# Kernel tuning notes

Measured on AMD Instinct MI355X. Metric: run time of the kernel, lower is better.

The kernel has to match this reference:

```python
import jax, jax.numpy as jnp
import numpy as np

Z, Y, X = 32, 480, 480          # sparse voxel grid (LiDAR-scale)
N = 200_000                     # active voxels
C_IN, C_OUT = 64, 64
EPS = 1e-5


def _subm_conv(f, nbr, w):
    """Submanifold sparse conv as gather-matmul-accumulate.
    f: [N, Cin]; nbr: [N, K] neighbor row ids, pad index == N for missing;
    w: [K, Cin, Cout]."""
    f_pad = jnp.concatenate([f, jnp.zeros((1, f.shape[1]), f.dtype)], axis=0)
    g = f_pad[nbr]                       # [N, K, Cin] gathered neighbor features
    return jnp.einsum('nkc,kco->no', g, w)


def _bn(x, gamma, beta):
    # BatchNorm1d in training mode: batch stats over the N dimension
    m = x.mean(axis=0)
    v = x.var(axis=0)
    return (x - m) * jax.lax.rsqrt(v + EPS) * gamma + beta


def setup_inputs() -> dict:
    rng = np.random.default_rng(0)
    ids = rng.choice(Z * Y * X, size=N, replace=False)
    lookup = np.full(Z * Y * X, -1, dtype=np.int64)
    lookup[ids] = np.arange(N)
    z = ids // (Y * X)
    y = (ids // X) % Y
    x = ids % X

    def nbr_table(offsets):
        cols = []
        for dz, dy, dx in offsets:
            zz, yy, xx = z + dz, y + dy, x + dx
            ok = (zz >= 0) & (zz < Z) & (yy >= 0) & (yy < Y) & (xx >= 0) & (xx < X)
            lin = np.clip((zz * Y + yy) * X + xx, 0, Z * Y * X - 1)
            idx = np.where(ok, lookup[lin], -1)
            cols.append(np.where(idx >= 0, idx, N))   # pad index N -> zero row
        return jnp.asarray(np.stack(cols, axis=1).astype(np.int32))

    off13 = [(0, dy, dx) for dy in (-1, 0, 1) for dx in (-1, 0, 1)]  # kernel (1,3,3)
    off31 = [(dz, 0, dx) for dz in (-1, 0, 1) for dx in (-1, 0, 1)]  # kernel (3,1,3)

    key = jax.random.key(0)
    ks = jax.random.split(key, 5)
    s = 0.05
    ones = jnp.ones((C_OUT,), jnp.float32)
    zeros = jnp.zeros((C_OUT,), jnp.float32)
    return {
        'features': jax.random.normal(ks[0], (N, C_IN), jnp.float32),
        'w1':   jax.random.normal(ks[1], (9, C_IN, C_OUT), jnp.float32) * s,
        'w1_2': jax.random.normal(ks[2], (9, C_OUT, C_OUT), jnp.float32) * s,
        'w2':   jax.random.normal(ks[3], (9, C_IN, C_OUT), jnp.float32) * s,
        'w3':   jax.random.normal(ks[4], (9, C_OUT, C_OUT), jnp.float32) * s,
        'g0': ones, 'b0': zeros, 'g0_2': ones, 'b0_2': zeros,
        'g1': ones, 'b1': zeros, 'g2': ones, 'b2': zeros,
        'nbr13': nbr_table(off13),
        'nbr31': nbr_table(off31),
    }


def reference(features, w1, w1_2, w2, w3, g0, b0, g0_2, b0_2, g1, b1, g2, b2,
              nbr13, nbr31):
    # shortcut branch: conv1x3 -> LeakyReLU -> BN -> conv3x1 -> LeakyReLU -> BN
    sc = _subm_conv(features, nbr13, w1)
    sc = _bn(jax.nn.leaky_relu(sc), g0, b0)
    sc = _subm_conv(sc, nbr31, w1_2)
    sc = _bn(jax.nn.leaky_relu(sc), g0_2, b0_2)
    # main branch: conv3x1 -> LeakyReLU -> BN -> conv1x3 -> LeakyReLU -> BN
    r = _subm_conv(features, nbr31, w2)
    r = _bn(jax.nn.leaky_relu(r), g1, b1)
    r = _subm_conv(r, nbr13, w3)
    r = _bn(jax.nn.leaky_relu(r), g2, b2)
    return r + sc
```

## Files before the change

kernel.cpp:

```cpp
#include <hip/hip_runtime.h>

#define NVOX 200000
#define TM 128
#define NBLK 1563
#define NREP 32
#define STG 4224

typedef unsigned short u16;
typedef unsigned int u32;
typedef __bf16 bf16x8 __attribute__((ext_vector_type(8)));
typedef float f32x16 __attribute__((ext_vector_type(16)));

__device__ __forceinline__ float bf2f(u16 h) { return __uint_as_float(((u32)h) << 16); }
__device__ __forceinline__ u16 f2bf(float x) {
  u32 u = __float_as_uint(x);
  u32 r = u + 0x7fffu + ((u >> 16) & 1u);
  return (u16)(r >> 16);
}
__device__ __forceinline__ uint4 cvt8(uint4 a, uint4 b) {
  const float* fa = (const float*)&a;
  const float* fb = (const float*)&b;
  uint4 r;
  u16* q = (u16*)&r;
#pragma unroll
  for (int j = 0; j < 4; ++j) { q[j] = f2bf(fa[j]); q[4 + j] = f2bf(fb[j]); }
  return r;
}

template <bool IN_F32, bool FOLDED, int MODE>
__global__ __launch_bounds__(256, 4)
void conv_k(const void* __restrict__ fv, const int* __restrict__ nbr,
            const u16* __restrict__ wf, void* yv, float* __restrict__ st,
            float* io, const float* __restrict__ affD,
            const float* __restrict__ affB) {
  __shared__ __align__(16) float fb[128 * 68];
  __shared__ float sred[4][128];

  const int tid = threadIdx.x;
  const int wv = tid >> 6;
  const int lane = tid & 63;
  const int lrow = lane & 31;
  const int lq = lane >> 5;
  const int base = blockIdx.x * TM;
  const int gr = base + wv * 32 + lrow;

  int ids[9];
#pragma unroll
  for (int j = 0; j < 9; ++j) ids[j] = (gr < NVOX) ? nbr[gr * 9 + j] : NVOX;

  f32x16 acc0 = {0.f, 0.f, 0.f, 0.f, 0.f, 0.f, 0.f, 0.f,
                 0.f, 0.f, 0.f, 0.f, 0.f, 0.f, 0.f, 0.f};
  f32x16 acc1 = acc0;
  constexpr int KSTRIDE = FOLDED ? 5120 : 4096;

#pragma unroll
  for (int k = 0; k < 9; ++k) {
    if (k != 4) {
      if (__ballot(ids[k] < NVOX) == 0ull) continue;
    }
    const int id = ids[k];
    const bool ok = id < NVOX;
    uint4 af[4];
    if constexpr (IN_F32) {
      const float* p = (const float*)fv + (size_t)id * 64 + lq * 8;
#pragma unroll
      for (int ksi = 0; ksi < 4; ++ksi) {
        uint4 v0 = make_uint4(0u, 0u, 0u, 0u), v1 = v0;
        if (ok) { v0 = *(const uint4*)(p + ksi * 16); v1 = *(const uint4*)(p + ksi * 16 + 4); }
        af[ksi] = cvt8(v0, v1);
      }
    } else {
      const u16* p = (const u16*)fv + (size_t)id * 64 + lq * 8;
#pragma unroll
      for (int ksi = 0; ksi < 4; ++ksi) {
        uint4 v = make_uint4(0u, 0u, 0u, 0u);
        if (ok) v = *(const uint4*)(p + ksi * 16);
        af[ksi] = v;
      }
    }
    const u16* wb = wf + k * KSTRIDE;
#pragma unroll
    for (int ksi = 0; ksi < 4; ++ksi) {
      bf16x8 a = __builtin_bit_cast(bf16x8, af[ksi]);
      bf16x8 b0 = __builtin_bit_cast(bf16x8, *(const uint4*)(wb + (ksi * 2) * 512 + lane * 8));
      bf16x8 b1 = __builtin_bit_cast(bf16x8, *(const uint4*)(wb + (ksi * 2 + 1) * 512 + lane * 8));
      acc0 = __builtin_amdgcn_mfma_f32_32x32x16_bf16(a, b0, acc0, 0, 0, 0);
      acc1 = __builtin_amdgcn_mfma_f32_32x32x16_bf16(a, b1, acc1, 0, 0, 0);
    }
    if constexpr (FOLDED) {
      uint4 a4 = make_uint4(0u, 0u, 0u, 0u);
      if (lq == 0 && ok) ((u16*)&a4)[0] = 0x3F80u;
      bf16x8 a = __builtin_bit_cast(bf16x8, a4);
      bf16x8 b0 = __builtin_bit_cast(bf16x8, *(const uint4*)(wb + 8 * 512 + lane * 8));
      bf16x8 b1 = __builtin_bit_cast(bf16x8, *(const uint4*)(wb + 9 * 512 + lane * 8));
      acc0 = __builtin_amdgcn_mfma_f32_32x32x16_bf16(a, b0, acc0, 0, 0, 0);
      acc1 = __builtin_amdgcn_mfma_f32_32x32x16_bf16(a, b1, acc1, 0, 0, 0);
    }
  }

  const int cc0 = lrow, cc1 = 32 + lrow;
  float aD0 = 0.f, aD1 = 0.f, hD0 = 0.f, hD1 = 0.f;
  if constexpr (MODE == 2) {
    aD0 = affD[cc0]; hD0 = affD[64 + cc0];
    aD1 = affD[cc1]; hD1 = affD[64 + cc1];
  }
  float s0 = 0.f, q0 = 0.f, s1 = 0.f, q1 = 0.f;
  float vout[2][16];
#pragma unroll
  for (int r = 0; r < 16; ++r) {
    float v = acc0[r]; v = v > 0.f ? v : 0.01f * v;
    s0 += v; q0 += v * v; vout[0][r] = v;
    float w = acc1[r]; w = w > 0.f ? w : 0.01f * w;
    s1 += w; q1 += w * w; vout[1][r] = w;
  }
  if constexpr (MODE != 2) {
    s0 += __shfl_xor(s0, 32); q0 += __shfl_xor(q0, 32);
    s1 += __shfl_xor(s1, 32); q1 += __shfl_xor(q1, 32);
    if (lq == 0) {
      sred[wv][lrow] = s0; sred[wv][32 + lrow] = s1;
      sred[wv][64 + lrow] = q0; sred[wv][96 + lrow] = q1;
    }
  }
  if constexpr (MODE == 0) {
    u16* bb = (u16*)fb;
#pragma unroll
    for (int r = 0; r < 16; ++r) {
      int rowD = 32 * wv + (r & 3) + 8 * (r >> 2) + 4 * lq;
      bb[rowD * 72 + cc0] = f2bf(vout[0][r]);
      bb[rowD * 72 + cc1] = f2bf(vout[1][r]);
    }
  } else if constexpr (MODE == 2 || MODE == 3) {
#pragma unroll
    for (int r = 0; r < 16; ++r) {
      int rowD = 32 * wv + (r & 3) + 8 * (r >> 2) + 4 * lq;
      float v0 = vout[0][r], v1 = vout[1][r];
      if constexpr (MODE == 2) { v0 = fmaf(v0, aD0, hD0); v1 = fmaf(v1, aD1, hD1); }
      fb[rowD * 68 + cc0] = v0;
      fb[rowD * 68 + cc1] = v1;
    }
  }
  __syncthreads();

  const int trow = tid >> 3, cp = tid & 7;
  if constexpr (MODE == 0) {
    u16* y = (u16*)yv;
    const u16* bb = (const u16*)fb;
#pragma unroll
    for (int it = 0; it < 4; ++it) {
      int r = it * 32 + trow, row = base + r;
      if (row < NVOX)
        *(uint4*)(y + (size_t)row * 64 + cp * 8) = *(const uint4*)(bb + r * 72 + cp * 8);
    }
  }
  if constexpr (MODE == 3) {
    float* y = (float*)yv;
#pragma unroll
    for (int it = 0; it < 4; ++it) {
      int r = it * 32 + trow, row = base + r;
      if (row < NVOX) {
        *(float4*)(y + (size_t)row * 64 + cp * 8) = *(const float4*)(fb + r * 68 + cp * 8);
        *(float4*)(y + (size_t)row * 64 + cp * 8 + 4) = *(const float4*)(fb + r * 68 + cp * 8 + 4);
      }
    }
  }
  if constexpr (MODE == 2) {
    float* y = (float*)yv;
#pragma unroll
    for (int it = 0; it < 4; ++it) {
      int r = it * 32 + trow, row = base + r;
      if (row < NVOX) {
        float t[8], p[8], o[8];
        *(float4*)&t[0] = *(const float4*)(fb + r * 68 + cp * 8);
        *(float4*)&t[4] = *(const float4*)(fb + r * 68 + cp * 8 + 4);
        *(float4*)&p[0] = *(const float4*)(io + (size_t)row * 64 + cp * 8);
        *(float4*)&p[4] = *(const float4*)(io + (size_t)row * 64 + cp * 8 + 4);
#pragma unroll
        for (int j = 0; j < 8; ++j) {
          int c = cp * 8 + j;
          o[j] = t[j] + fmaf(p[j], affB[c], affB[64 + c]);
        }
        *(float4*)(y + (size_t)row * 64 + cp * 8) = *(const float4*)&o[0];
        *(float4*)(y + (size_t)row * 64 + cp * 8 + 4) = *(const float4*)&o[4];
      }
    }
  }
  if constexpr (MODE != 2) {
    if (tid < 128) {
      int which = tid >> 6, c = tid & 63;
      float v = sred[0][which * 64 + c] + sred[1][which * 64 + c] +
                sred[2][which * 64 + c] + sred[3][which * 64 + c];
      atomicAdd(&st[(blockIdx.x & (NREP - 1)) * 128 + which * 64 + c], v);
    }
  }
}

__global__ void prep_all(const float* __restrict__ feat, const float* __restrict__ w1,
                         const float* __restrict__ w2, u16* __restrict__ wf,
                         u16* __restrict__ F, float* __restrict__ st, int cvt_blocks) {
  const int bid = blockIdx.x, tid = threadIdx.x;
  if (bid < cvt_blocks) {
    int i8 = (bid * 256 + tid) * 8;
    if (i8 < NVOX * 64) {
      uint4 a = *(const uint4*)(feat + i8);
      uint4 b = *(const uint4*)(feat + i8 + 4);
      *(uint4*)(F + i8) = cvt8(a, b);
    }
    return;
  }
  int rb = bid - cvt_blocks;
  if (rb < 288) {
    int e = rb * 256 + tid;
    int slot = e / 36864, r = e % 36864;
    int k = r >> 12, rr = r & 4095;
    int frag = rr >> 9, lane = (rr >> 3) & 63, j = rr & 7;
    int ks = frag >> 1, ct = frag & 1;
    int cin = ks * 16 + (lane >> 5) * 8 + j;
    int cout = ct * 32 + (lane & 31);
    const float* src = slot ? w2 : w1;
    wf[e] = f2bf(src[k * 4096 + cin * 64 + cout]);
    return;
  }
  for (int i = tid; i < 4 * STG; i += 256) st[i] = 0.f;
}

__global__ void wscale(const float* __restrict__ wraw, float* __restrict__ stp,
                       const float* __restrict__ g, const float* __restrict__ b,
                       u16* __restrict__ dst) {
  __shared__ float sc[64], sh[64];
  const int tid = threadIdx.x;
  if (tid < 64) {
    float s = 0.f, q = 0.f;
#pragma unroll
    for (int r = 0; r < NREP; ++r) {
      s += stp[r * 128 + tid];
      q += stp[r * 128 + 64 + tid];
    }
    const float invn = 1.0f / (float)NVOX;
    float mean = s * invn;
    float var = q * invn - mean * mean;
    float sca = g[tid] * rsqrtf(var + 1e-5f);
    sc[tid] = sca;
    sh[tid] = b[tid] - mean * sca;
    if (blockIdx.x == 0) { stp[4096 + tid] = sca; stp[4160 + tid] = sh[tid]; }
  }
  __syncthreads();
  int e = blockIdx.x * 256 + tid;
  int k = e / 5120, r = e % 5120;
  int frag = r >> 9, lane = (r >> 3) & 63, j = r & 7;
  int ks = frag >> 1, ct = frag & 1;
  int cout = ct * 32 + (lane & 31);
  u16 val = 0;
  if (ks < 4) {
    int cin = ks * 16 + (lane >> 5) * 8 + j;
    val = f2bf(sc[cin] * wraw[k * 4096 + cin * 64 + cout]);
  } else if (((lane >> 5) == 0) && j == 0) {
    float acc = 0.f;
    for (int c = 0; c < 64; ++c) acc += sh[c] * wraw[k * 4096 + c * 64 + cout];
    val = f2bf(acc);
  }
  dst[e] = val;
}

__global__ void finalize_bn(float* __restrict__ st, const float* __restrict__ g,
                            const float* __restrict__ b) {
  int c = threadIdx.x;
  if (c < 64) {
    float s = 0.f, q = 0.f;
#pragma unroll
    for (int r = 0; r < NREP; ++r) {
      s += st[r * 128 + c];
      q += st[r * 128 + 64 + c];
    }
    const float invn = 1.0f / (float)NVOX;
    float mean = s * invn;
    float var = q * invn - mean * mean;
    float sca = g[c] * rsqrtf(var + 1e-5f);
    st[4096 + c] = sca;
    st[4160 + c] = b[c] - mean * sca;
  }
}

__global__ void final_add(const u16* __restrict__ y3, float* io,
                          const float* __restrict__ affB, const float* __restrict__ affD) {
  int i8 = (blockIdx.x * 256 + threadIdx.x) * 8;
  if (i8 < NVOX * 64) {
    float a[8];
    *(float4*)&a[0] = *(const float4*)(io + i8);
    *(float4*)&a[4] = *(const float4*)(io + i8 + 4);
    uint4 vd = *(const uint4*)(y3 + i8);
    const u16* pd = (const u16*)&vd;
    int cb = i8 & 63;
    float o[8];
#pragma unroll
    for (int j = 0; j < 8; ++j) {
      int c = cb + j;
      o[j] = fmaf(a[j], affB[c], affB[64 + c]) + fmaf(bf2f(pd[j]), affD[c], affD[64 + c]);
    }
    *(float4*)(io + i8) = *(const float4*)&o[0];
    *(float4*)(io + i8 + 4) = *(const float4*)&o[4];
  }
}

extern "C" void kernel_launch(void* const* d_in, const int* in_sizes, int n_in,
                              void* d_out, int out_size, void* d_ws, size_t ws_size,
                              hipStream_t stream) {
  const float* feat = (const float*)d_in[0];
  const float* w1 = (const float*)d_in[1];
  const float* w1_2 = (const float*)d_in[2];
  const float* w2 = (const float*)d_in[3];
  const float* w3 = (const float*)d_in[4];
  const float* g0 = (const float*)d_in[5];
  const float* b0 = (const float*)d_in[6];
  const float* g0_2 = (const float*)d_in[7];
  const float* b0_2 = (const float*)d_in[8];
  const float* g1 = (const float*)d_in[9];
  const float* b1 = (const float*)d_in[10];
  const float* g2 = (const float*)d_in[11];
  const float* b2 = (const float*)d_in[12];
  const int* nbr13 = (const int*)d_in[13];
  const int* nbr31 = (const int*)d_in[14];
  float* out = (float*)d_out;

  char* ws = (char*)d_ws;
  float* st = (float*)ws;
  u16* wf = (u16*)(ws + 67584);
  u16* s0 = wf;
  u16* s1 = wf + 36864;
  u16* s2 = wf + 73728;
  u16* s3 = wf + 119808;
  u16* F = (u16*)(ws + 67584 + 331776);
  u16* A = F + (size_t)NVOX * 64;
  const size_t need_big = 67584 + 331776 + 2ull * NVOX * 64 * 2;
  const bool big = (ws_size >= need_big);

  float* st0 = st, *st1 = st + STG, *st2 = st + 2 * STG, *st3 = st + 3 * STG;

  if (big) {
    prep_all<<<6539, 256, 0, stream>>>(feat, w1, w2, wf, F, st, 6250);
    conv_k<false, false, 0><<<NBLK, 256, 0, stream>>>(F, nbr13, s0, A, st0, nullptr, nullptr, nullptr);
    wscale<<<180, 256, 0, stream>>>(w1_2, st0, g0, b0, s2);
    conv_k<false, true, 3><<<NBLK, 256, 0, stream>>>(A, nbr31, s2, out, st1, nullptr, nullptr, nullptr);
    conv_k<false, false, 0><<<NBLK, 256, 0, stream>>>(F, nbr31, s1, A, st2, nullptr, nullptr, nullptr);
    wscale<<<180, 256, 0, stream>>>(w3, st2, g1, b1, s3);
    conv_k<false, true, 0><<<NBLK, 256, 0, stream>>>(A, nbr13, s3, F, st3, nullptr, nullptr, nullptr);
    finalize_bn<<<1, 64, 0, stream>>>(st1, g0_2, b0_2);
    finalize_bn<<<1, 64, 0, stream>>>(st3, g2, b2);
    final_add<<<6250, 256, 0, stream>>>(F, out, st1 + 4096, st3 + 4096);
  } else {
    u16* Az = F;
    prep_all<<<289, 256, 0, stream>>>(feat, w1, w2, wf, nullptr, st, 0);
    conv_k<true, false, 0><<<NBLK, 256, 0, stream>>>(feat, nbr13, s0, Az, st0, nullptr, nullptr, nullptr);
    wscale<<<180, 256, 0, stream>>>(w1_2, st0, g0, b0, s2);
    conv_k<false, true, 3><<<NBLK, 256, 0, stream>>>(Az, nbr31, s2, out, st1, nullptr, nullptr, nullptr);
    finalize_bn<<<1, 64, 0, stream>>>(st1, g0_2, b0_2);
    conv_k<true, false, 0><<<NBLK, 256, 0, stream>>>(feat, nbr31, s1, Az, st2, nullptr, nullptr, nullptr);
    wscale<<<180, 256, 0, stream>>>(w3, st2, g1, b1, s3);
    conv_k<false, true, 1><<<NBLK, 256, 0, stream>>>(Az, nbr13, s3, nullptr, st3, nullptr, nullptr, nullptr);
    finalize_bn<<<1, 64, 0, stream>>>(st3, g2, b2);
    conv_k<false, true, 2><<<NBLK, 256, 0, stream>>>(Az, nbr13, s3, out, nullptr, out, st3 + 4096, st1 + 4096);
  }
}
```

Baseline: 287.6 us.

## Fuse independent branch convolutions into single launches with doubled grid

Adds a conv_fused kernel that runs the shortcut and main branch convolutions of the same stage in one launch, with blocks split by index between the two branches. It also merges the two weight-scaling kernels and the two BN finalizers, and doubles the stats replica count to spread atomic contention. The aim is fewer launches, more concurrent work per launch and less serialization between stages. The cost is a third activation buffer, a larger workspace, and a new fused kernel that drops early-exit and epilogue variants. The fallback paths call wscale2 with mismatched grid sizes and fragile ordering.

```diff
diff --git a/kernel.cpp b/kernel.cpp
--- a/kernel.cpp
+++ b/kernel.cpp
@@ -3,8 +3,8 @@
 #define NVOX 200000
 #define TM 128
 #define NBLK 1563
-#define NREP 32
-#define STG 4224
+#define NREP 64
+#define STG 8320
 
 typedef unsigned short u16;
 typedef unsigned int u32;
@@ -25,6 +25,142 @@
 #pragma unroll
   for (int j = 0; j < 4; ++j) { q[j] = f2bf(fa[j]); q[4 + j] = f2bf(fb[j]); }
   return r;
+}
+
+template <int PHASE>
+__global__ __launch_bounds__(256, 4)
+void conv_fused(const u16* __restrict__ inA, const u16* __restrict__ inB,
+                const int* __restrict__ nbrA, const int* __restrict__ nbrB,
+                const u16* __restrict__ wfA, const u16* __restrict__ wfB,
+                void* yA, void* yB, float* __restrict__ stA, float* __restrict__ stB) {
+  __shared__ __align__(16) float fb4[64 * 68];
+  __shared__ float sred[4][128];
+
+  const int tid = threadIdx.x;
+  const int bid = blockIdx.x;
+  const bool hB = (bid >= NBLK);
+  const int blk = hB ? bid - NBLK : bid;
+  const u16* f = hB ? inB : inA;
+  const int* nbr = hB ? nbrB : nbrA;
+  const u16* wf = hB ? wfB : wfA;
+  float* st = hB ? stB : stA;
+
+  const int wv = tid >> 6;
+  const int lane = tid & 63;
+  const int lrow = lane & 31;
+  const int lq = lane >> 5;
+  const int base = blk * TM;
+  const int gr = base + wv * 32 + lrow;
+
+  int ids[9];
+#pragma unroll
+  for (int j = 0; j < 9; ++j) ids[j] = (gr < NVOX) ? nbr[gr * 9 + j] : NVOX;
+
+  f32x16 acc0 = {0.f, 0.f, 0.f, 0.f, 0.f, 0.f, 0.f, 0.f,
+                 0.f, 0.f, 0.f, 0.f, 0.f, 0.f, 0.f, 0.f};
+  f32x16 acc1 = acc0;
+  constexpr bool FOLDED = (PHASE == 1);
+  constexpr int KSTRIDE = FOLDED ? 5120 : 4096;
+
+#pragma unroll
+  for (int k = 0; k < 9; ++k) {
+    if (k != 4) {
+      if (__ballot(ids[k] < NVOX) == 0ull) continue;
+    }
+    const int id = ids[k];
+    const bool ok = id < NVOX;
+    uint4 af[4];
+    const u16* p = f + (size_t)id * 64 + lq * 8;
+#pragma unroll
+    for (int ksi = 0; ksi < 4; ++ksi) {
+      uint4 v = make_uint4(0u, 0u, 0u, 0u);
+      if (ok) v = *(const uint4*)(p + ksi * 16);
+      af[ksi] = v;
+    }
+    const u16* wb = wf + k * KSTRIDE;
+#pragma unroll
+    for (int ksi = 0; ksi < 4; ++ksi) {
+      bf16x8 a = __builtin_bit_cast(bf16x8, af[ksi]);
+      bf16x8 b0 = __builtin_bit_cast(bf16x8, *(const uint4*)(wb + (ksi * 2) * 512 + lane * 8));
+      bf16x8 b1 = __builtin_bit_cast(bf16x8, *(const uint4*)(wb + (ksi * 2 + 1) * 512 + lane * 8));
+      acc0 = __builtin_amdgcn_mfma_f32_32x32x16_bf16(a, b0, acc0, 0, 0, 0);
+      acc1 = __builtin_amdgcn_mfma_f32_32x32x16_bf16(a, b1, acc1, 0, 0, 0);
+    }
+    if constexpr (FOLDED) {
+      uint4 a4 = make_uint4(0u, 0u, 0u, 0u);
+      if (lq == 0 && ok) ((u16*)&a4)[0] = 0x3F80u;
+      bf16x8 a = __builtin_bit_cast(bf16x8, a4);
+      bf16x8 b0 = __builtin_bit_cast(bf16x8, *(const uint4*)(wb + 8 * 512 + lane * 8));
+      bf16x8 b1 = __builtin_bit_cast(bf16x8, *(const uint4*)(wb + 9 * 512 + lane * 8));
+      acc0 = __builtin_amdgcn_mfma_f32_32x32x16_bf16(a, b0, acc0, 0, 0, 0);
+      acc1 = __builtin_amdgcn_mfma_f32_32x32x16_bf16(a, b1, acc1, 0, 0, 0);
+    }
+  }
+
+  const int cc0 = lrow, cc1 = 32 + lrow;
+  float s0 = 0.f, q0 = 0.f, s1 = 0.f, q1 = 0.f;
+  float vout[2][16];
+#pragma unroll
+  for (int r = 0; r < 16; ++r) {
+    float v = acc0[r]; v = v > 0.f ? v : 0.01f * v;
+    s0 += v; q0 += v * v; vout[0][r] = v;
+    float w = acc1[r]; w = w > 0.f ? w : 0.01f * w;
+    s1 += w; q1 += w * w; vout[1][r] = w;
+  }
+  s0 += __shfl_xor(s0, 32); q0 += __shfl_xor(q0, 32);
+  s1 += __shfl_xor(s1, 32); q1 += __shfl_xor(q1, 32);
+  if (lq == 0) {
+    sred[wv][lrow] = s0; sred[wv][32 + lrow] = s1;
+    sred[wv][64 + lrow] = q0; sred[wv][96 + lrow] = q1;
+  }
+
+  const bool f32out = (PHASE == 1) && !hB;
+  const int trow = tid >> 3, cp = tid & 7;
+  u16* bb = (u16*)fb4;
+#pragma unroll
+  for (int h = 0; h < 2; ++h) {
+    __syncthreads();
+    if ((wv >> 1) == h) {
+      const int lr = 32 * (wv & 1);
+#pragma unroll
+      for (int r = 0; r < 16; ++r) {
+        int rowD = lr + (r & 3) + 8 * (r >> 2) + 4 * lq;
+        if (f32out) {
+          fb4[rowD * 68 + cc0] = vout[0][r];
+          fb4[rowD * 68 + cc1] = vout[1][r];
+        } else {
+          bb[rowD * 72 + cc0] = f2bf(vout[0][r]);
+          bb[rowD * 72 + cc1] = f2bf(vout[1][r]);
+        }
+      }
+    }
+    __syncthreads();
+    if (f32out) {
+      float* y = (float*)yA;
+#pragma unroll
+      for (int it = 0; it < 2; ++it) {
+        int r = it * 32 + trow, row = base + 64 * h + r;
+        if (row < NVOX) {
+          *(float4*)(y + (size_t)row * 64 + cp * 8) = *(const float4*)(fb4 + r * 68 + cp * 8);
+          *(float4*)(y + (size_t)row * 64 + cp * 8 + 4) = *(const float4*)(fb4 + r * 68 + cp * 8 + 4);
+        }
+      }
+    } else {
+      u16* y = (u16*)(hB ? yB : yA);
+#pragma unroll
+      for (int it = 0; it < 2; ++it) {
+        int r = it * 32 + trow, row = base + 64 * h + r;
+        if (row < NVOX)
+          *(uint4*)(y + (size_t)row * 64 + cp * 8) = *(const uint4*)(bb + r * 72 + cp * 8);
+      }
+    }
+  }
+  if (tid < 128) {
+    int which = tid >> 6, c = tid & 63;
+    float v = sred[0][which * 64 + c] + sred[1][which * 64 + c] +
+              sred[2][which * 64 + c] + sred[3][which * 64 + c];
+    atomicAdd(&st[(bid & (NREP - 1)) * 128 + which * 64 + c], v);
+  }
 }
 
 template <bool IN_F32, bool FOLDED, int MODE>
@@ -223,28 +359,46 @@
   for (int i = tid; i < 4 * STG; i += 256) st[i] = 0.f;
 }
 
-__global__ void wscale(const float* __restrict__ wraw, float* __restrict__ stp,
-                       const float* __restrict__ g, const float* __restrict__ b,
-                       u16* __restrict__ dst) {
+__device__ __forceinline__ void bn_from_replicas(const float* stp, const float* g,
+                                                 const float* b, int c,
+                                                 float* sc, float* sh) {
+  float s = 0.f, q = 0.f;
+#pragma unroll
+  for (int r = 0; r < NREP; ++r) {
+    s += stp[r * 128 + c];
+    q += stp[r * 128 + 64 + c];
+  }
+  const float invn = 1.0f / (float)NVOX;
+  float mean = s * invn;
+  float var = q * invn - mean * mean;
+  float sca = g[c] * rsqrtf(var + 1e-5f);
+  *sc = sca;
+  *sh = b[c] - mean * sca;
+}
+
+__global__ void wscale2(const float* __restrict__ wA, float* __restrict__ stpA,
+                        const float* __restrict__ gA, const float* __restrict__ bA,
+                        u16* __restrict__ dA,
+                        const float* __restrict__ wB, float* __restrict__ stpB,
+                        const float* __restrict__ gB, const float* __restrict__ bB,
+                        u16* __restrict__ dB) {
   __shared__ float sc[64], sh[64];
   const int tid = threadIdx.x;
+  const bool hB = (blockIdx.x >= 180);
+  const float* wraw = hB ? wB : wA;
+  float* stp = hB ? stpB : stpA;
+  const float* g = hB ? gB : gA;
+  const float* b = hB ? bB : bA;
+  u16* dst = hB ? dB : dA;
+  const int blk = hB ? blockIdx.x - 180 : blockIdx.x;
   if (tid < 64) {
-    float s = 0.f, q = 0.f;
-#pragma unroll
-    for (int r = 0; r < NREP; ++r) {
-      s += stp[r * 128 + tid];
-      q += stp[r * 128 + 64 + tid];
-    }
-    const float invn = 1.0f / (float)NVOX;
-    float mean = s * invn;
-    float var = q * invn - mean * mean;
-    float sca = g[tid] * rsqrtf(var + 1e-5f);
-    sc[tid] = sca;
-    sh[tid] = b[tid] - mean * sca;
-    if (blockIdx.x == 0) { stp[4096 + tid] = sca; stp[4160 + tid] = sh[tid]; }
+    float a, h;
+    bn_from_replicas(stp, g, b, tid, &a, &h);
+    sc[tid] = a; sh[tid] = h;
+    if (blk == 0) { stp[NREP * 128 + tid] = a; stp[NREP * 128 + 64 + tid] = h; }
   }
   __syncthreads();
-  int e = blockIdx.x * 256 + tid;
+  int e = blk * 256 + tid;
   int k = e / 5120, r = e % 5120;
   int frag = r >> 9, lane = (r >> 3) & 63, j = r & 7;
   int ks = frag >> 1, ct = frag & 1;
@@ -261,22 +415,19 @@
   dst[e] = val;
 }
 
-__global__ void finalize_bn(float* __restrict__ st, const float* __restrict__ g,
-                            const float* __restrict__ b) {
-  int c = threadIdx.x;
-  if (c < 64) {
-    float s = 0.f, q = 0.f;
-#pragma unroll
-    for (int r = 0; r < NREP; ++r) {
-      s += st[r * 128 + c];
-      q += st[r * 128 + 64 + c];
-    }
-    const float invn = 1.0f / (float)NVOX;
-    float mean = s * invn;
-    float var = q * invn - mean * mean;
-    float sca = g[c] * rsqrtf(var + 1e-5f);
-    st[4096 + c] = sca;
-    st[4160 + c] = b[c] - mean * sca;
+__global__ void finalize2(float* __restrict__ stA, const float* __restrict__ gA,
+                          const float* __restrict__ bA, float* __restrict__ stB,
+                          const float* __restrict__ gB, const float* __restrict__ bB) {
+  int t = threadIdx.x;
+  float* stp = (t < 64) ? stA : stB;
+  const float* g = (t < 64) ? gA : gB;
+  const float* b = (t < 64) ? bA : bB;
+  int c = t & 63;
+  if (t < 128) {
+    float a, h;
+    bn_from_replicas(stp, g, b, c, &a, &h);
+    stp[NREP * 128 + c] = a;
+    stp[NREP * 128 + 64 + c] = h;
   }
 }
 
@@ -323,40 +474,51 @@
 
   char* ws = (char*)d_ws;
   float* st = (float*)ws;
-  u16* wf = (u16*)(ws + 67584);
+  u16* wf = (u16*)(ws + 133120);
   u16* s0 = wf;
   u16* s1 = wf + 36864;
   u16* s2 = wf + 73728;
   u16* s3 = wf + 119808;
-  u16* F = (u16*)(ws + 67584 + 331776);
-  u16* A = F + (size_t)NVOX * 64;
-  const size_t need_big = 67584 + 331776 + 2ull * NVOX * 64 * 2;
-  const bool big = (ws_size >= need_big);
+  u16* F = (u16*)(ws + 133120 + 331776);
+  u16* A1 = F + (size_t)NVOX * 64;
+  u16* A2 = A1 + (size_t)NVOX * 64;
+  const size_t base_sz = 133120 + 331776;
+  const size_t need_fused = base_sz + 3ull * NVOX * 64 * 2;
+  const size_t need_serial = base_sz + 2ull * NVOX * 64 * 2;
 
   float* st0 = st, *st1 = st + STG, *st2 = st + 2 * STG, *st3 = st + 3 * STG;
 
-  if (big) {
+  if (ws_size >= need_fused) {
     prep_all<<<6539, 256, 0, stream>>>(feat, w1, w2, wf, F, st, 6250);
-    conv_k<false, false, 0><<<NBLK, 256, 0, stream>>>(F, nbr13, s0, A, st0, nullptr, nullptr, nullptr);
-    wscale<<<180, 256, 0, stream>>>(w1_2, st0, g0, b0, s2);
-    conv_k<false, true, 3><<<NBLK, 256, 0, stream>>>(A, nbr31, s2, out, st1, nullptr, nullptr, nullptr);
-    conv_k<false, false, 0><<<NBLK, 256, 0, stream>>>(F, nbr31, s1, A, st2, nullptr, nullptr, nullptr);
-    wscale<<<180, 256, 0, stream>>>(w3, st2, g1, b1, s3);
-    conv_k<false, true, 0><<<NBLK, 256, 0, stream>>>(A, nbr13, s3, F, st3, nullptr, nullptr, nullptr);
-    finalize_bn<<<1, 64, 0, stream>>>(st1, g0_2, b0_2);
-    finalize_bn<<<1, 64, 0, stream>>>(st3, g2, b2);
-    final_add<<<6250, 256, 0, stream>>>(F, out, st1 + 4096, st3 + 4096);
+    conv_fused<0><<<2 * NBLK, 256, 0, stream>>>(F, F, nbr13, nbr31, s0, s1,
+                                                A1, A2, st0, st2);
+    wscale2<<<360, 256, 0, stream>>>(w1_2, st0, g0, b0, s2, w3, st2, g1, b1, s3);
+    conv_fused<1><<<2 * NBLK, 256, 0, stream>>>(A1, A2, nbr31, nbr13, s2, s3,
+                                                out, F, st1, st3);
+    finalize2<<<1, 128, 0, stream>>>(st1, g0_2, b0_2, st3, g2, b2);
+    final_add<<<6250, 256, 0, stream>>>(F, out, st1 + NREP * 128, st3 + NREP * 128);
+  } else if (ws_size >= need_serial) {
+    prep_all<<<6539, 256, 0, stream>>>(feat, w1, w2, wf, F, st, 6250);
+    conv_k<false, false, 0><<<NBLK, 256, 0, stream>>>(F, nbr13, s0, A1, st0, nullptr, nullptr, nullptr);
+    wscale2<<<180, 256, 0, stream>>>(w1_2, st0, g0, b0, s2, w3, st2, g1, b1, s3);
+    conv_k<false, true, 3><<<NBLK, 256, 0, stream>>>(A1, nbr31, s2, out, st1, nullptr, nullptr, nullptr);
+    conv_k<false, false, 0><<<NBLK, 256, 0, stream>>>(F, nbr31, s1, A1, st2, nullptr, nullptr, nullptr);
+    wscale2<<<360, 256, 0, stream>>>(w1_2, st0, g0, b0, s2, w3, st2, g1, b1, s3);
+    conv_k<false, true, 0><<<NBLK, 256, 0, stream>>>(A1, nbr13, s3, F, st3, nullptr, nullptr, nullptr);
+    finalize2<<<1, 128, 0, stream>>>(st1, g0_2, b0_2, st3, g2, b2);
+    final_add<<<6250, 256, 0, stream>>>(F, out, st1 + NREP * 128, st3 + NREP * 128);
   } else {
     u16* Az = F;
     prep_all<<<289, 256, 0, stream>>>(feat, w1, w2, wf, nullptr, st, 0);
     conv_k<true, false, 0><<<NBLK, 256, 0, stream>>>(feat, nbr13, s0, Az, st0, nullptr, nullptr, nullptr);
-    wscale<<<180, 256, 0, stream>>>(w1_2, st0, g0, b0, s2);
+    wscale2<<<180, 256, 0, stream>>>(w1_2, st0, g0, b0, s2, w3, st2, g1, b1, s3);
     conv_k<false, true, 3><<<NBLK, 256, 0, stream>>>(Az, nbr31, s2, out, st1, nullptr, nullptr, nullptr);
-    finalize_bn<<<1, 64, 0, stream>>>(st1, g0_2, b0_2);
+    finalize2<<<1, 128, 0, stream>>>(st1, g0_2, b0_2, st3, g2, b2);
     conv_k<true, false, 0><<<NBLK, 256, 0, stream>>>(feat, nbr31, s1, Az, st2, nullptr, nullptr, nullptr);
-    wscale<<<180, 256, 0, stream>>>(w3, st2, g1, b1, s3);
+    wscale2<<<360, 256, 0, stream>>>(w1_2, st0, g0, b0, s2, w3, st2, g1, b1, s3);
     conv_k<false, true, 1><<<NBLK, 256, 0, stream>>>(Az, nbr13, s3, nullptr, st3, nullptr, nullptr, nullptr);
-    finalize_bn<<<1, 64, 0, stream>>>(st3, g2, b2);
-    conv_k<false, true, 2><<<NBLK, 256, 0, stream>>>(Az, nbr13, s3, out, nullptr, out, st3 + 4096, st1 + 4096);
-  }
-}
+    finalize2<<<1, 128, 0, stream>>>(st1, g0_2, b0_2, st3, g2, b2);
+    conv_k<false, true, 2><<<NBLK, 256, 0, stream>>>(Az, nbr13, s3, out, nullptr, out,
+                                                     st3 + NREP * 128, st1 + NREP * 128);
+  }
+}
```

Result: faster. 261.6 us (-9.0%).
